# Performance work log

Measured on AMD Instinct MI355X. Metric: run time of the kernel, lower is better.

## Reference

```python
import jax, jax.numpy as jnp
import numpy as np

N_NODES = 100000
N_EDGES = 1000000
D = 256


def setup_inputs() -> dict:
    key = jax.random.key(0)
    ks = jax.random.split(key, 5)
    h = jax.random.normal(ks[0], (N_NODES, D), dtype=jnp.float32)
    edges = jax.random.randint(ks[1], (N_EDGES, 2), 0, N_NODES, dtype=jnp.int64)
    # xavier-uniform-style linear weights, stored as [in, out]
    def xavier(k, fan_in, fan_out):
        limit = float(np.sqrt(6.0 / (fan_in + fan_out)))
        return jax.random.uniform(k, (fan_in, fan_out), dtype=jnp.float32, minval=-limit, maxval=limit)
    W1 = xavier(ks[2], D, D // 2)
    W2 = xavier(ks[3], D // 2, D // 4)
    W3 = xavier(ks[4], D // 4, 2)
    return {
        "h": h, "edges": edges,
        "W1": W1, "b1": jnp.zeros((D // 2,), jnp.float32),
        "W2": W2, "b2": jnp.zeros((D // 4,), jnp.float32),
        "W3": W3, "b3": jnp.zeros((2,), jnp.float32),
    }


def reference(h, edges, W1, b1, W2, b2, W3, b3):
    # gather endpoint embeddings and combine via hadamard product: [E, D]
    emb = h[edges[:, 0]] * h[edges[:, 1]]
    # small MLP chain 256 -> 128 -> 64 -> 2
    out = emb @ W1 + b1
    out = out @ W2 + b2
    out = out @ W3 + b3
    # softmax over class dim
    return jax.nn.softmax(out, axis=1)
```

## Files before the change

### kernel.cpp

```cpp
#include <hip/hip_runtime.h>
#include <hip/hip_bf16.h>


#define D 256

typedef _Float16 half8 __attribute__((ext_vector_type(8)));
typedef float float4v __attribute__((ext_vector_type(4)));

__global__ __launch_bounds__(256) void prep(
    const float4* __restrict__ h, half8* __restrict__ tb, int nv8,
    const float* __restrict__ W1, const float* __restrict__ b1,
    const float* __restrict__ W2, const float* __restrict__ b2,
    const float* __restrict__ W3, const float* __restrict__ b3,
    float* __restrict__ wc, _Float16* __restrict__ wdf)
{
    if (blockIdx.x == 0) {
        __shared__ float T[128][2];
        const int t = threadIdx.x;
        {
            const int j = t >> 1, c = t & 1;
            float s = 0.f;
            #pragma unroll 8
            for (int k = 0; k < 64; ++k) s += W2[j * 64 + k] * W3[k * 2 + c];
            T[j][c] = s;
        }
        __syncthreads();
        float s0 = 0.f, s1 = 0.f;
        #pragma unroll 8
        for (int j = 0; j < 128; ++j) {
            const float w = W1[t * 128 + j];
            s0 += w * T[j][0];
            s1 += w * T[j][1];
        }
        const float wd = s1 - s0;
        wc[t]  = wd;
        wdf[t] = (_Float16)wd;
        if (t == 0) {
            float f0 = b3[0], f1 = b3[1];
            for (int j = 0; j < 128; ++j) { f0 += b1[j] * T[j][0]; f1 += b1[j] * T[j][1]; }
            for (int k = 0; k < 64; ++k)  { f0 += b2[k] * W3[k * 2 + 0]; f1 += b2[k] * W3[k * 2 + 1]; }
            wc[256] = f1 - f0;
        }
    }

    const int gstride = gridDim.x * blockDim.x;
    for (int i = blockIdx.x * blockDim.x + threadIdx.x; i < nv8; i += gstride) {
        const float4 f0 = h[2 * i];
        const float4 f1 = h[2 * i + 1];
        half8 o;
        o[0] = (_Float16)f0.x; o[1] = (_Float16)f0.y;
        o[2] = (_Float16)f0.z; o[3] = (_Float16)f0.w;
        o[4] = (_Float16)f1.x; o[5] = (_Float16)f1.y;
        o[6] = (_Float16)f1.z; o[7] = (_Float16)f1.w;
        tb[i] = o;
    }
}

__global__ __launch_bounds__(256) void edge_mfma(
    const _Float16* __restrict__ tbl, const int2* __restrict__ edges,
    const float* __restrict__ wc, const _Float16* __restrict__ wdf,
    float2* __restrict__ out, int E, int ngroups)
{
    const int lane = threadIdx.x & 63;
    const int m    = lane & 15;
    const int quad = lane >> 4;
    const int wid  = blockIdx.x * (blockDim.x >> 6) + (threadIdx.x >> 6);
    const int nw   = gridDim.x * (blockDim.x >> 6);

    const float bd = wc[256];
    const bool diag = (quad == (m >> 2));

    half8 wq[8];
    {
        const half8* wp = (const half8*)(wdf + quad * 8);
        #pragma unroll
        for (int s = 0; s < 8; ++s) wq[s] = wp[4 * s];
    }

    for (int g = wid; g < ngroups; g += nw) {
        const int em = g * 16 + m;
        const int2 ed = edges[min(em, E - 1)];
        const half8* pa = (const half8*)(tbl + (size_t)ed.x * D + quad * 8);
        const half8* pb = (const half8*)(tbl + (size_t)ed.y * D + quad * 8);

        float4v acc = {0.f, 0.f, 0.f, 0.f};
        #pragma unroll
        for (int s = 0; s < 8; ++s) {
            const half8 a = pa[4 * s] * wq[s];
            const half8 b = pb[4 * s];
            acc = __builtin_amdgcn_mfma_f32_16x16x32_f16(a, b, acc, 0, 0, 0);
        }

        if (diag && em < E) {
            const float d  = acc[m & 3] + bd;
            const float p1 = 1.0f / (1.0f + __expf(-d));
            out[em] = make_float2(1.0f - p1, p1);
        }
    }
}

__global__ __launch_bounds__(256) void edge_predict_f32(
    const float* __restrict__ h, const int2* __restrict__ edges,
    const float* __restrict__ wc, float2* __restrict__ out, int E)
{
    const int lane = threadIdx.x & 63;
    const int wid  = blockIdx.x * (blockDim.x >> 6) + (threadIdx.x >> 6);
    const int nw   = gridDim.x * (blockDim.x >> 6);
    const float4 wd = ((const float4*)wc)[lane];
    const float  bd = wc[256];
    for (int e = wid; e < E; e += nw) {
        const int2 ed = edges[e];
        const float4 a = ((const float4*)(h + (size_t)ed.x * D))[lane];
        const float4 b = ((const float4*)(h + (size_t)ed.y * D))[lane];
        float d = a.x * b.x * wd.x + a.y * b.y * wd.y + a.z * b.z * wd.z + a.w * b.w * wd.w;
        #pragma unroll
        for (int mm = 32; mm > 0; mm >>= 1) d += __shfl_xor(d, mm, 64);
        if (lane == 0) {
            const float p1 = 1.0f / (1.0f + __expf(-(d + bd)));
            out[e] = make_float2(1.0f - p1, p1);
        }
    }
}

extern "C" void kernel_launch(void* const* d_in, const int* in_sizes, int n_in,
                              void* d_out, int out_size, void* d_ws, size_t ws_size,
                              hipStream_t stream)
{
    const float* h     = (const float*)d_in[0];
    const int2*  edges = (const int2*)d_in[1];
    const float* W1    = (const float*)d_in[2];
    const float* b1    = (const float*)d_in[3];
    const float* W2    = (const float*)d_in[4];
    const float* b2    = (const float*)d_in[5];
    const float* W3    = (const float*)d_in[6];
    const float* b3    = (const float*)d_in[7];
    float2* out = (float2*)d_out;

    const int nNodes = in_sizes[0] / D;
    const int E      = in_sizes[1] / 2;

    float*     wc  = (float*)d_ws;
    _Float16*  wdf = (_Float16*)((char*)d_ws + 1280);
    _Float16*  tbl = (_Float16*)((char*)d_ws + 2048);
    const size_t need = 2048 + (size_t)nNodes * D * 2;

    if (ws_size >= need) {
        const int nv8 = nNodes * (D / 8);
        prep<<<4096, 256, 0, stream>>>((const float4*)h, (half8*)tbl, nv8,
                                       W1, b1, W2, b2, W3, b3, wc, wdf);
        const int ngroups = (E + 15) / 16;
        edge_mfma<<<2048, 256, 0, stream>>>(tbl, edges, wc, wdf, out, E, ngroups);
    } else {
        prep<<<1, 256, 0, stream>>>((const float4*)h, (half8*)wc , 0,
                                    W1, b1, W2, b2, W3, b3, wc, wdf);
        edge_predict_f32<<<2048, 256, 0, stream>>>(h, edges, wc, out, E);
    }
}
```

Before: 315.7 us.

## Counting-sort edges by source node before the MFMA edge kernel

Adds a per-call counting sort of edges by source node: the histogram is zeroed inside prep, then a histogram, a two-level scan and an atomic scatter produce a permuted edge list with original indices. The MFMA kernel then walks contiguous chunks of sorted edges, so consecutive groups reuse the same source row from cache instead of gathering random rows. This aims to cut gather traffic on the fp16 node table. In exchange it adds four extra launches, global atomics and a scattered output write through the index array, and it needs more workspace, falling back to the old path if that is missing.

```diff
diff --git a/kernel.cpp b/kernel.cpp
--- a/kernel.cpp
+++ b/kernel.cpp
@@ -12,8 +12,13 @@
     const float* __restrict__ W1, const float* __restrict__ b1,
     const float* __restrict__ W2, const float* __restrict__ b2,
     const float* __restrict__ W3, const float* __restrict__ b3,
-    float* __restrict__ wc, _Float16* __restrict__ wdf)
-{
+    float* __restrict__ wc, _Float16* __restrict__ wdf,
+    int* __restrict__ hist, int nhp)
+{
+    const int gstride = gridDim.x * blockDim.x;
+    for (int i = blockIdx.x * blockDim.x + threadIdx.x; i < nhp; i += gstride)
+        hist[i] = 0;
+
     if (blockIdx.x == 0) {
         __shared__ float T[128][2];
         const int t = threadIdx.x;
@@ -43,7 +48,6 @@
         }
     }
 
-    const int gstride = gridDim.x * blockDim.x;
     for (int i = blockIdx.x * blockDim.x + threadIdx.x; i < nv8; i += gstride) {
         const float4 f0 = h[2 * i];
         const float4 f1 = h[2 * i + 1];
@@ -53,6 +57,120 @@
         o[4] = (_Float16)f1.x; o[5] = (_Float16)f1.y;
         o[6] = (_Float16)f1.z; o[7] = (_Float16)f1.w;
         tb[i] = o;
+    }
+}
+
+__global__ __launch_bounds__(256) void hist_k(
+    const int2* __restrict__ edges, int* __restrict__ hist, int E)
+{
+    const int gstride = gridDim.x * blockDim.x;
+    for (int e = blockIdx.x * blockDim.x + threadIdx.x; e < E; e += gstride)
+        atomicAdd(&hist[edges[e].x], 1);
+}
+
+__global__ __launch_bounds__(256) void scan1(
+    const int* __restrict__ in, int* __restrict__ outp, int* __restrict__ aux, int n)
+{
+    __shared__ int buf[2][256];
+    const int t = threadIdx.x;
+    const int gid = blockIdx.x * 256 + t;
+    const int v = (gid < n) ? in[gid] : 0;
+    buf[0][t] = v;
+    __syncthreads();
+    int src = 0;
+    for (int off = 1; off < 256; off <<= 1) {
+        int val = buf[src][t];
+        if (t >= off) val += buf[src][t - off];
+        buf[src ^ 1][t] = val;
+        src ^= 1;
+        __syncthreads();
+    }
+    if (gid < n) outp[gid] = buf[src][t] - v;
+    if (t == 255) aux[blockIdx.x] = buf[src][t];
+}
+
+__global__ __launch_bounds__(256) void scan2(int* __restrict__ aux, int n)
+{
+    __shared__ int buf[2][256];
+    const int t = threadIdx.x;
+    int v[4];
+    const int base = t * 4;
+    for (int k = 0; k < 4; ++k) { const int i = base + k; v[k] = (i < n) ? aux[i] : 0; }
+    const int local = v[0] + v[1] + v[2] + v[3];
+    buf[0][t] = local;
+    __syncthreads();
+    int src = 0;
+    for (int off = 1; off < 256; off <<= 1) {
+        int val = buf[src][t];
+        if (t >= off) val += buf[src][t - off];
+        buf[src ^ 1][t] = val;
+        src ^= 1;
+        __syncthreads();
+    }
+    int run = buf[src][t] - local;
+    for (int k = 0; k < 4; ++k) { const int i = base + k; if (i < n) aux[i] = run; run += v[k]; }
+}
+
+__global__ __launch_bounds__(256) void scatter_k(
+    const int2* __restrict__ edges, int* __restrict__ cursor,
+    const int* __restrict__ aux, int2* __restrict__ puv,
+    int* __restrict__ pidx, int E)
+{
+    const int gstride = gridDim.x * blockDim.x;
+    for (int e = blockIdx.x * blockDim.x + threadIdx.x; e < E; e += gstride) {
+        const int2 ed = edges[e];
+        const int pos = atomicAdd(&cursor[ed.x], 1) + aux[ed.x >> 8];
+        puv[pos] = ed;
+        pidx[pos] = e;
+    }
+}
+
+__global__ __launch_bounds__(256) void edge_mfma_sorted(
+    const _Float16* __restrict__ tbl, const int2* __restrict__ puv,
+    const int* __restrict__ pidx, const float* __restrict__ wc,
+    const _Float16* __restrict__ wdf, float2* __restrict__ out,
+    int E, int chunk)
+{
+    const int lane = threadIdx.x & 63;
+    const int m    = lane & 15;
+    const int quad = lane >> 4;
+    const int wid  = blockIdx.x * (blockDim.x >> 6) + (threadIdx.x >> 6);
+
+    const int s0 = wid * chunk;
+    if (s0 >= E) return;
+    const int eend = min(E, s0 + chunk);
+
+    const float bd = wc[256];
+    const bool diag = (quad == (m >> 2));
+
+    half8 wq[8];
+    {
+        const half8* wp = (const half8*)(wdf + quad * 8);
+        #pragma unroll
+        for (int s = 0; s < 8; ++s) wq[s] = wp[4 * s];
+    }
+
+    for (int g = s0; g < eend; g += 16) {
+        const int em = g + m;
+        const bool valid = (em < eend);
+        const int ec = valid ? em : (eend - 1);
+        const int2 ed = puv[ec];
+        const half8* pa = (const half8*)(tbl + (size_t)ed.x * D + quad * 8);
+        const half8* pb = (const half8*)(tbl + (size_t)ed.y * D + quad * 8);
+
+        float4v acc = {0.f, 0.f, 0.f, 0.f};
+        #pragma unroll
+        for (int s = 0; s < 8; ++s) {
+            const half8 a = pa[4 * s] * wq[s];
+            const half8 b = pb[4 * s];
+            acc = __builtin_amdgcn_mfma_f32_16x16x32_f16(a, b, acc, 0, 0, 0);
+        }
+
+        if (diag && valid) {
+            const float d  = acc[m & 3] + bd;
+            const float p1 = 1.0f / (1.0f + __expf(-d));
+            out[pidx[em]] = make_float2(1.0f - p1, p1);
+        }
     }
 }
 
@@ -138,21 +256,44 @@
 
     const int nNodes = in_sizes[0] / D;
     const int E      = in_sizes[1] / 2;
-
-    float*     wc  = (float*)d_ws;
-    _Float16*  wdf = (_Float16*)((char*)d_ws + 1280);
-    _Float16*  tbl = (_Float16*)((char*)d_ws + 2048);
-    const size_t need = 2048 + (size_t)nNodes * D * 2;
-
-    if (ws_size >= need) {
-        const int nv8 = nNodes * (D / 8);
+    const int nv8    = nNodes * (D / 8);
+
+    const int    nblk1 = (nNodes + 255) / 256;
+    const int    nhp   = nblk1 * 256;
+
+    char* p = (char*)d_ws;
+    float*    wc  = (float*)p;
+    _Float16* wdf = (_Float16*)(p + 1280);
+    _Float16* tbl = (_Float16*)(p + 2048);
+    p += 2048 + (size_t)nNodes * D * 2;
+    const size_t needTbl = (size_t)(p - (char*)d_ws);
+    int2* puv    = (int2*)p;  p += (size_t)E * 8;
+    int*  pidx   = (int*)p;   p += (size_t)E * 4;
+    int*  hist   = (int*)p;   p += (size_t)nhp * 4;
+    int*  cursor = (int*)p;   p += (size_t)nhp * 4;
+    int*  aux    = (int*)p;   p += 4096;
+    const size_t needSort = (size_t)(p - (char*)d_ws);
+
+    if (ws_size >= needSort && nblk1 <= 1024) {
         prep<<<4096, 256, 0, stream>>>((const float4*)h, (half8*)tbl, nv8,
-                                       W1, b1, W2, b2, W3, b3, wc, wdf);
+                                       W1, b1, W2, b2, W3, b3, wc, wdf, hist, nhp);
+        hist_k<<<2048, 256, 0, stream>>>(edges, hist, E);
+        scan1<<<nblk1, 256, 0, stream>>>(hist, cursor, aux, nNodes);
+        scan2<<<1, 256, 0, stream>>>(aux, nblk1);
+        scatter_k<<<2048, 256, 0, stream>>>(edges, cursor, aux, puv, pidx, E);
+        const int nw = 2048 * 4;
+        int chunk = (E + nw - 1) / nw;
+        chunk = (chunk + 15) & ~15;
+        edge_mfma_sorted<<<2048, 256, 0, stream>>>(tbl, puv, pidx, wc, wdf,
+                                                   out, E, chunk);
+    } else if (ws_size >= needTbl) {
+        prep<<<4096, 256, 0, stream>>>((const float4*)h, (half8*)tbl, nv8,
+                                       W1, b1, W2, b2, W3, b3, wc, wdf, hist, 0);
         const int ngroups = (E + 15) / 16;
         edge_mfma<<<2048, 256, 0, stream>>>(tbl, edges, wc, wdf, out, E, ngroups);
     } else {
         prep<<<1, 256, 0, stream>>>((const float4*)h, (half8*)wc , 0,
-                                    W1, b1, W2, b2, W3, b3, wc, wdf);
+                                    W1, b1, W2, b2, W3, b3, wc, wdf, hist, 0);
         edge_predict_f32<<<2048, 256, 0, stream>>>(h, edges, wc, out, E);
     }
 }
```

Result: slower. 398.4 us (+26.2%).

## Bin edges by source node so each wave reuses the source embedding row

Applied to the files above, without the earlier changes.

Adds a binfill pass that uses atomic counters to bucket edges by source node into fixed slots of up to 14, with overflow going to a spill list. The new edge kernel then handles two source nodes per wave, loading each source row once and gathering only the destination rows for up to 16 edges. The aim is to roughly halve random-gather traffic on the fp16 table. The cost is an extra atomic-heavy pass, slot-array writes, idle MFMA lanes for under-filled bins, and edges silently dropped if spill exceeds its cap.

```diff
diff --git a/kernel.cpp b/kernel.cpp
--- a/kernel.cpp
+++ b/kernel.cpp
@@ -3,6 +3,8 @@
 
 
 #define D 256
+#define NSLOT 14
+#define SPILLCAP 32768
 
 typedef _Float16 half8 __attribute__((ext_vector_type(8)));
 typedef float float4v __attribute__((ext_vector_type(4)));
@@ -12,8 +14,13 @@
     const float* __restrict__ W1, const float* __restrict__ b1,
     const float* __restrict__ W2, const float* __restrict__ b2,
     const float* __restrict__ W3, const float* __restrict__ b3,
-    float* __restrict__ wc, _Float16* __restrict__ wdf)
-{
+    float* __restrict__ wc, _Float16* __restrict__ wdf,
+    int* __restrict__ cursor, int ncur)
+{
+    const int gstride = gridDim.x * blockDim.x;
+    for (int i = blockIdx.x * blockDim.x + threadIdx.x; i < ncur; i += gstride)
+        cursor[i] = 0;
+
     if (blockIdx.x == 0) {
         __shared__ float T[128][2];
         const int t = threadIdx.x;
@@ -43,7 +50,6 @@
         }
     }
 
-    const int gstride = gridDim.x * blockDim.x;
     for (int i = blockIdx.x * blockDim.x + threadIdx.x; i < nv8; i += gstride) {
         const float4 f0 = h[2 * i];
         const float4 f1 = h[2 * i + 1];
@@ -56,10 +62,29 @@
     }
 }
 
-__global__ __launch_bounds__(256) void edge_mfma(
-    const _Float16* __restrict__ tbl, const int2* __restrict__ edges,
-    const float* __restrict__ wc, const _Float16* __restrict__ wdf,
-    float2* __restrict__ out, int E, int ngroups)
+__global__ __launch_bounds__(256) void binfill(
+    const int2* __restrict__ edges, int* __restrict__ cursor,
+    int* __restrict__ spillcnt, int2* __restrict__ slots,
+    int4* __restrict__ spill, int E)
+{
+    const int gstride = gridDim.x * blockDim.x;
+    for (int e = blockIdx.x * blockDim.x + threadIdx.x; e < E; e += gstride) {
+        const int2 ed = edges[e];
+        const int pos = atomicAdd(&cursor[ed.x], 1);
+        if (pos < NSLOT) {
+            slots[(size_t)ed.x * NSLOT + pos] = make_int2(ed.y, e);
+        } else {
+            const int s = atomicAdd(spillcnt, 1);
+            if (s < SPILLCAP) spill[s] = make_int4(ed.x, ed.y, e, 0);
+        }
+    }
+}
+
+__global__ __launch_bounds__(256) void edge_binned(
+    const _Float16* __restrict__ tbl, const int2* __restrict__ slots,
+    const int* __restrict__ cursor, const int* __restrict__ spillcnt,
+    const int4* __restrict__ spill, const float* __restrict__ wc,
+    const _Float16* __restrict__ wdf, float2* __restrict__ out, int NB)
 {
     const int lane = threadIdx.x & 63;
     const int m    = lane & 15;
@@ -68,6 +93,88 @@
     const int nw   = gridDim.x * (blockDim.x >> 6);
 
     const float bd = wc[256];
+
+    half8 wq[8];
+    {
+        const half8* wp = (const half8*)(wdf + quad * 8);
+        #pragma unroll
+        for (int s = 0; s < 8; ++s) wq[s] = wp[4 * s];
+    }
+
+    for (int b = wid * 2; b < NB; b += nw * 2) {
+        const int b2ok = (b + 1 < NB);
+        const int bb2  = b2ok ? b + 1 : b;
+        const int f1 = min(cursor[b], NSLOT);
+        const int f2 = b2ok ? min(cursor[bb2], NSLOT) : 0;
+        if ((f1 | f2) == 0) continue;
+
+        const int ms = min(m, NSLOT - 1);
+        const int2 r1 = slots[(size_t)b   * NSLOT + ms];
+        const int2 r2 = slots[(size_t)bb2 * NSLOT + ms];
+        const int v1 = (m < f1) ? r1.x : 0;
+        const int v2 = (m < f2) ? r2.x : 0;
+
+        const half8* pa1 = (const half8*)(tbl + (size_t)b   * D + quad * 8);
+        const half8* pa2 = (const half8*)(tbl + (size_t)bb2 * D + quad * 8);
+        const half8* pb1 = (const half8*)(tbl + (size_t)v1  * D + quad * 8);
+        const half8* pb2 = (const half8*)(tbl + (size_t)v2  * D + quad * 8);
+
+        float4v acc1 = {0.f, 0.f, 0.f, 0.f};
+        float4v acc2 = {0.f, 0.f, 0.f, 0.f};
+        #pragma unroll
+        for (int s = 0; s < 8; ++s) {
+            acc1 = __builtin_amdgcn_mfma_f32_16x16x32_f16(pa1[4 * s] * wq[s], pb1[4 * s], acc1, 0, 0, 0);
+            acc2 = __builtin_amdgcn_mfma_f32_16x16x32_f16(pa2[4 * s] * wq[s], pb2[4 * s], acc2, 0, 0, 0);
+        }
+
+        if (quad == 0) {
+            if (m < f1) {
+                const float p = 1.0f / (1.0f + __expf(-(acc1[0] + bd)));
+                out[r1.y] = make_float2(1.0f - p, p);
+            }
+            if (m < f2) {
+                const float p = 1.0f / (1.0f + __expf(-(acc2[0] + bd)));
+                out[r2.y] = make_float2(1.0f - p, p);
+            }
+        }
+    }
+
+    const int nspill = min(*spillcnt, SPILLCAP);
+    if (nspill > 0) {
+        const int ngroups = (nspill + 15) >> 4;
+        const bool diag = (quad == (m >> 2));
+        for (int g = wid; g < ngroups; g += nw) {
+            const int i = g * 16 + m;
+            const bool valid = (i < nspill);
+            const int4 sp = spill[min(i, nspill - 1)];
+            const int uu = valid ? sp.x : 0;
+            const int vv = valid ? sp.y : 0;
+            const half8* pa = (const half8*)(tbl + (size_t)uu * D + quad * 8);
+            const half8* pb = (const half8*)(tbl + (size_t)vv * D + quad * 8);
+            float4v acc = {0.f, 0.f, 0.f, 0.f};
+            #pragma unroll
+            for (int s = 0; s < 8; ++s)
+                acc = __builtin_amdgcn_mfma_f32_16x16x32_f16(pa[4 * s] * wq[s], pb[4 * s], acc, 0, 0, 0);
+            if (diag && valid) {
+                const float p = 1.0f / (1.0f + __expf(-(acc[m & 3] + bd)));
+                out[sp.z] = make_float2(1.0f - p, p);
+            }
+        }
+    }
+}
+
+__global__ __launch_bounds__(256) void edge_mfma(
+    const _Float16* __restrict__ tbl, const int2* __restrict__ edges,
+    const float* __restrict__ wc, const _Float16* __restrict__ wdf,
+    float2* __restrict__ out, int E, int ngroups)
+{
+    const int lane = threadIdx.x & 63;
+    const int m    = lane & 15;
+    const int quad = lane >> 4;
+    const int wid  = blockIdx.x * (blockDim.x >> 6) + (threadIdx.x >> 6);
+    const int nw   = gridDim.x * (blockDim.x >> 6);
+
+    const float bd = wc[256];
     const bool diag = (quad == (m >> 2));
 
     half8 wq[8];
@@ -85,16 +192,12 @@
 
         float4v acc = {0.f, 0.f, 0.f, 0.f};
         #pragma unroll
-        for (int s = 0; s < 8; ++s) {
-            const half8 a = pa[4 * s] * wq[s];
-            const half8 b = pb[4 * s];
-            acc = __builtin_amdgcn_mfma_f32_16x16x32_f16(a, b, acc, 0, 0, 0);
-        }
+        for (int s = 0; s < 8; ++s)
+            acc = __builtin_amdgcn_mfma_f32_16x16x32_f16(pa[4 * s] * wq[s], pb[4 * s], acc, 0, 0, 0);
 
         if (diag && em < E) {
-            const float d  = acc[m & 3] + bd;
-            const float p1 = 1.0f / (1.0f + __expf(-d));
-            out[em] = make_float2(1.0f - p1, p1);
+            const float p = 1.0f / (1.0f + __expf(-(acc[m & 3] + bd)));
+            out[em] = make_float2(1.0f - p, p);
         }
     }
 }
@@ -138,21 +241,40 @@
 
     const int nNodes = in_sizes[0] / D;
     const int E      = in_sizes[1] / 2;
-
-    float*     wc  = (float*)d_ws;
-    _Float16*  wdf = (_Float16*)((char*)d_ws + 1280);
-    _Float16*  tbl = (_Float16*)((char*)d_ws + 2048);
-    const size_t need = 2048 + (size_t)nNodes * D * 2;
-
-    if (ws_size >= need) {
-        const int nv8 = nNodes * (D / 8);
+    const int nv8    = nNodes * (D / 8);
+
+    char* p = (char*)d_ws;
+    float*    wc  = (float*)p;
+    _Float16* wdf = (_Float16*)(p + 1280);
+    _Float16* tbl = (_Float16*)(p + 2048);
+    p += 2048 + (size_t)nNodes * D * 2;
+    const size_t needTbl = (size_t)(p - (char*)d_ws);
+    int* cursor = (int*)p;
+    const int ncur = nNodes + 16;
+    int* spillcnt = cursor + nNodes;
+    p += ((size_t)ncur * 4 + 15) & ~(size_t)15;
+    int2* slots = (int2*)p;   p += (size_t)nNodes * NSLOT * 8;
+    int4* spill = (int4*)p;   p += (size_t)SPILLCAP * 16;
+    const size_t needBin = (size_t)(p - (char*)d_ws);
+
+    if (ws_size >= needBin) {
         prep<<<4096, 256, 0, stream>>>((const float4*)h, (half8*)tbl, nv8,
-                                       W1, b1, W2, b2, W3, b3, wc, wdf);
+                                       W1, b1, W2, b2, W3, b3, wc, wdf,
+                                       cursor, ncur);
+        binfill<<<2048, 256, 0, stream>>>(edges, cursor, spillcnt, slots,
+                                          spill, E);
+        edge_binned<<<2048, 256, 0, stream>>>(tbl, slots, cursor, spillcnt,
+                                              spill, wc, wdf, out, nNodes);
+    } else if (ws_size >= needTbl) {
+        prep<<<4096, 256, 0, stream>>>((const float4*)h, (half8*)tbl, nv8,
+                                       W1, b1, W2, b2, W3, b3, wc, wdf,
+                                       cursor, 0);
         const int ngroups = (E + 15) / 16;
         edge_mfma<<<2048, 256, 0, stream>>>(tbl, edges, wc, wdf, out, E, ngroups);
     } else {
         prep<<<1, 256, 0, stream>>>((const float4*)h, (half8*)wc , 0,
-                                    W1, b1, W2, b2, W3, b3, wc, wdf);
+                                    W1, b1, W2, b2, W3, b3, wc, wdf,
+                                    cursor, 0);
         edge_predict_f32<<<2048, 256, 0, stream>>>(h, edges, wc, out, E);
     }
 }
```

After: 392.8 us. 1.24x slower.
